# Kernel optimization log

Measured on AMD Instinct MI355X. Metric: run time of the kernel, lower is better.

Reference implementation:

```python
import jax, jax.numpy as jnp
import numpy as np

BS, SL, CL = 32, 512, 20      # batch, seq_len (visits), codes per visit
D, H, V = 256, 4, 20000       # d_model, heads, vocab_size
HD = D // H                   # size_per_head = 64
EPS = 1e-5


def make_pe_table(d_model, max_pos):
    # torch PositionalEncoding: sinusoidal table with a zero pad row prepended
    pe = np.array([[pos / np.power(10000, 2.0 * (j // 2) / d_model)
                    for j in range(d_model)] for pos in range(max_pos)])
    pe[:, 0::2] = np.sin(pe[:, 0::2])
    pe[:, 1::2] = np.cos(pe[:, 1::2])
    pe = np.concatenate([np.zeros((1, d_model)), pe], axis=0)
    return jnp.asarray(pe, dtype=jnp.float32)  # [max_pos+1, d]


def layer_norm(x, g, b):
    mu = jnp.mean(x, axis=-1, keepdims=True)
    var = jnp.mean(jnp.square(x - mu), axis=-1, keepdims=True)
    return (x - mu) * jax.lax.rsqrt(var + EPS) * g + b


def setup_inputs() -> dict:
    key = jax.random.key(0)
    ks = jax.random.split(key, 12)
    input_seqs = jax.random.randint(ks[0], (BS, SL, CL), 0, V, dtype=jnp.int32)
    masks = jnp.ones((BS, SL, SL), dtype=jnp.int32)
    lengths = jax.random.randint(ks[1], (BS,), 1, SL + 1, dtype=jnp.int32)
    seq_time_step = jax.random.uniform(ks[2], (BS, SL), dtype=jnp.float32)
    code_masks = jax.random.uniform(ks[3], (BS, SL, CL), dtype=jnp.float32)

    emb_table = jax.random.normal(ks[4], (V + 1, D), dtype=jnp.float32) * 0.02
    emb_table = emb_table.at[V].set(0.0)  # padding_idx row (never indexed here)
    bound = 1.0 / np.sqrt(V)
    bias_emb = jax.random.uniform(ks[5], (D,), minval=-bound, maxval=bound, dtype=jnp.float32)
    s = 1.0 / np.sqrt(D)
    Wq = jax.random.uniform(ks[6], (D, D), minval=-s, maxval=s, dtype=jnp.float32)
    Wk = jax.random.uniform(ks[7], (D, D), minval=-s, maxval=s, dtype=jnp.float32)
    Wv = jax.random.uniform(ks[8], (D, D), minval=-s, maxval=s, dtype=jnp.float32)
    Wfc = jax.random.uniform(ks[9], (D, D), minval=-s, maxval=s, dtype=jnp.float32)
    ln_g = jnp.ones((D,), dtype=jnp.float32)
    ln_b = jnp.zeros((D,), dtype=jnp.float32)
    so = 1.0 / np.sqrt(4 * D)
    out_w = jax.random.uniform(ks[10], (2, 4 * D), minval=-so, maxval=so, dtype=jnp.float32)
    out_b = jax.random.uniform(ks[11], (2,), minval=-so, maxval=so, dtype=jnp.float32)
    pe_table = make_pe_table(D, SL)

    return dict(input_seqs=input_seqs, masks=masks, lengths=lengths,
                seq_time_step=seq_time_step, code_masks=code_masks,
                emb_table=emb_table, bias_emb=bias_emb, pe_table=pe_table,
                Wq=Wq, Wk=Wk, Wv=Wv, Wfc=Wfc, ln_g=ln_g, ln_b=ln_b,
                out_w=out_w, out_b=out_b)


def reference(input_seqs, masks, lengths, seq_time_step, code_masks,
              emb_table, bias_emb, pe_table, Wq, Wk, Wv, Wfc,
              ln_g, ln_b, out_w, out_b):
    bs, sl, _ = input_seqs.shape
    # visit embedding: sum of code embeddings + bias  -> [bs, sl, d]
    x = emb_table[input_seqs].sum(axis=2) + bias_emb
    # positional encoding: pos ids = 1..len, 0 beyond length
    t_idx = jnp.arange(sl, dtype=jnp.int32)
    pos_ids = jnp.where(t_idx[None, :] < lengths[:, None], t_idx[None, :] + 1, 0)
    x = x + pe_table[pos_ids]
    res = x
    # manual MHA -- NOTE faithful to original: view(bs, H, sl, hd) directly
    q = (x @ Wq.T).reshape(bs, H, sl, HD)
    k = (x @ Wk.T).reshape(bs, H, sl, HD)
    v = (x @ Wv.T).reshape(bs, H, sl, HD)
    energy = jnp.einsum('bhqd,bhkd->bhqk', q, k) / np.sqrt(HD)
    energy = jnp.where(masks[:, None, :, :] == 0, -jnp.inf, energy)
    attn = jax.nn.softmax(energy, axis=-1)
    o = jnp.einsum('bhqk,bhkd->bhqd', attn, v)          # [bs,H,sl,hd]
    o = o.transpose(0, 2, 1, 3).reshape(bs, sl, D)
    x = layer_norm(o @ Wfc.T + res, ln_g, ln_b)
    # zero out positions >= length
    valid = (t_idx[None, :] < lengths[:, None])          # [bs, sl]
    x = jnp.where(valid[:, :, None], x, 0.0)
    # triangular-weighted temporal pooling into 4 bins (vectorized loops)
    lens = lengths.astype(jnp.float32)
    t = jnp.arange(1, sl + 1, dtype=jnp.float32)
    s_val = 4.0 * t[None, :] / lens[:, None]             # [bs, sl]
    m = jnp.arange(1, 5, dtype=jnp.float32)              # 4 bins
    w = jnp.square(1.0 - jnp.abs(s_val[:, :, None] - m[None, None, :]) / 4.0)  # [bs,sl,4]
    U = jnp.einsum('bsm,bsd->bmd', w, x)                 # [bs,4,d]
    U = U.reshape(bs, 4 * D)
    return U @ out_w.T + out_b                           # [bs, 2]
```

## Files before the change

kernel.cpp:

```cpp
#include <hip/hip_runtime.h>

#define BSZ 32
#define SLEN 512
#define CLEN 20
#define DMOD 256
#define NH 4
#define HDIM 64

typedef _Float16 half8 __attribute__((ext_vector_type(8)));
typedef _Float16 half4 __attribute__((ext_vector_type(4)));
typedef float float4v __attribute__((ext_vector_type(4)));

#define MFMA16(a, b, c) __builtin_amdgcn_mfma_f32_16x16x32_f16(a, b, c, 0, 0, 0)
#define PG(fi) ((((fi) >> 4) * 17) + ((fi) & 15))

__global__ __launch_bounds__(256) void k_cast(
    const float* __restrict__ W0, const float* __restrict__ W1,
    const float* __restrict__ W2, const float* __restrict__ W3,
    const float* __restrict__ emb,
    _Float16* __restrict__ wh, _Float16* __restrict__ embh) {
  const int bid = blockIdx.x;
  const float* src;
  _Float16* dst;
  int idx;
  if (bid < 128) {
    const int z = bid >> 5;
    src = (z == 0) ? W0 : (z == 1) ? W1 : (z == 2) ? W2 : W3;
    dst = wh + (size_t)z * 65536;
    idx = ((bid & 31) * 256 + threadIdx.x) * 8;
  } else {
    src = emb;
    dst = embh;
    idx = ((bid - 128) * 256 + threadIdx.x) * 8;
  }
  float v[8];
  *(float4*)v = *(const float4*)(src + idx);
  *(float4*)(v + 4) = *(const float4*)(src + idx + 4);
  half8 h;
  #pragma unroll
  for (int i = 0; i < 8; ++i) h[i] = (_Float16)v[i];
  *(half8*)(dst + idx) = h;
}

__global__ __launch_bounds__(256) void k_embmask(
    const int* __restrict__ seqs, const int* __restrict__ lengths,
    const _Float16* __restrict__ embh, const float* __restrict__ bias,
    const float* __restrict__ pe, _Float16* __restrict__ x,
    const int* __restrict__ masks, unsigned int* __restrict__ pk) {
  const int row0 = blockIdx.x * 8;
  const int sub = threadIdx.x >> 5;
  const int hl = threadIdx.x & 31;
  const int row = row0 + sub;
  const int b = row >> 9, s = row & 511;
  __shared__ int codes[8][CLEN];
  if (threadIdx.x < 8 * CLEN)
    codes[threadIdx.x / CLEN][threadIdx.x % CLEN] = seqs[row0 * CLEN + threadIdx.x];
  __syncthreads();
  const int pos = (s < lengths[b]) ? (s + 1) : 0;
  const int d = hl * 8;
  half8 ev[CLEN];
  #pragma unroll
  for (int c = 0; c < CLEN; ++c)
    ev[c] = *(const half8*)(embh + (size_t)codes[sub][c] * DMOD + d);
  float acc[8];
  *(float4*)acc = *(const float4*)(bias + d);
  *(float4*)(acc + 4) = *(const float4*)(bias + d + 4);
  const float4 pv0 = *(const float4*)(pe + (size_t)pos * DMOD + d);
  const float4 pv1 = *(const float4*)(pe + (size_t)pos * DMOD + d + 4);
  acc[0] += pv0.x; acc[1] += pv0.y; acc[2] += pv0.z; acc[3] += pv0.w;
  acc[4] += pv1.x; acc[5] += pv1.y; acc[6] += pv1.z; acc[7] += pv1.w;
  #pragma unroll
  for (int c = 0; c < CLEN; ++c) {
    #pragma unroll
    for (int i = 0; i < 8; ++i) acc[i] += (float)ev[c][i];
  }
  half8 hv;
  #pragma unroll
  for (int i = 0; i < 8; ++i) hv[i] = (_Float16)acc[i];
  *(half8*)(x + (size_t)row * DMOD + d) = hv;
  const int wv = threadIdx.x >> 6;
  const int lane = threadIdx.x & 63;
  int mv[16];
  #pragma unroll
  for (int p = 0; p < 16; ++p) {
    const int it = wv + p * 4;
    const int r = row0 + (it >> 3);
    const int chunk = it & 7;
    mv[p] = masks[(size_t)r * SLEN + chunk * 64 + lane];
  }
  #pragma unroll
  for (int p = 0; p < 16; ++p) {
    const int it = wv + p * 4;
    const int r = row0 + (it >> 3);
    const int chunk = it & 7;
    const unsigned long long bal = __ballot(mv[p] != 0);
    if (lane == 0) {
      pk[(size_t)r * 16 + chunk * 2]     = (unsigned int)bal;
      pk[(size_t)r * 16 + chunk * 2 + 1] = (unsigned int)(bal >> 32);
    }
  }
}

__global__ __launch_bounds__(256) void k_gemm_qkv(
    const _Float16* __restrict__ A, const _Float16* __restrict__ Wb,
    _Float16* __restrict__ q, _Float16* __restrict__ k, _Float16* __restrict__ v) {
  const int z = blockIdx.z;
  _Float16* Cb = (z == 0) ? q : (z == 1) ? k : v;
  const _Float16* w_ = Wb + (size_t)z * 65536;
  const int m0 = blockIdx.x * 128;
  const int n0 = blockIdx.y * 128;
  const int tid = threadIdx.x;
  const int lane = tid & 63;
  const int w = tid >> 6;
  const int wm = (w >> 1) * 4;
  const int wn = (w & 1) * 4;
  __shared__ _Float16 smem[8704];
  half8* As = (half8*)(smem);
  half8* Ws = (half8*)(smem + 4096);
  float4v acc[4][4];
  #pragma unroll
  for (int i = 0; i < 4; ++i)
    #pragma unroll
    for (int j = 0; j < 4; ++j)
      acc[i][j] = (float4v){0.f, 0.f, 0.f, 0.f};
  int li_[2]; size_t ga_[2], gw_[2];
  #pragma unroll
  for (int p = 0; p < 2; ++p) {
    const int c = tid + p * 256;
    const int r = c & 127, qd = c >> 7;
    li_[p] = (r >> 4) * 64 + qd * 16 + (r & 15);
    ga_[p] = (size_t)(m0 + r) * DMOD + qd * 8;
    gw_[p] = (size_t)(n0 + r) * DMOD + qd * 8;
  }
  half8 pa[2], pw[2];
  #pragma unroll
  for (int p = 0; p < 2; ++p) {
    pa[p] = *(const half8*)(A + ga_[p]);
    pw[p] = *(const half8*)(w_ + gw_[p]);
  }
  for (int k0 = 0; k0 < DMOD; k0 += 32) {
    #pragma unroll
    for (int p = 0; p < 2; ++p) {
      As[li_[p]] = pa[p];
      Ws[li_[p]] = pw[p];
    }
    __syncthreads();
    if (k0 + 32 < DMOD) {
      #pragma unroll
      for (int p = 0; p < 2; ++p) {
        pa[p] = *(const half8*)(A + ga_[p] + k0 + 32);
        pw[p] = *(const half8*)(w_ + gw_[p] + k0 + 32);
      }
    }
    half8 af[4], wf[4];
    #pragma unroll
    for (int i = 0; i < 4; ++i) {
      af[i] = As[(wm + i) * 64 + lane];
      wf[i] = Ws[(wn + i) * 64 + lane];
    }
    #pragma unroll
    for (int i = 0; i < 4; ++i)
      #pragma unroll
      for (int j = 0; j < 4; ++j)
        acc[i][j] = MFMA16(af[i], wf[j], acc[i][j]);
    __syncthreads();
  }
  const int cr = (lane >> 4) * 4;
  const int cc = lane & 15;
  _Float16* Eh = smem;
  #pragma unroll
  for (int ip = 0; ip < 4; ++ip) {
    #pragma unroll
    for (int j = 0; j < 4; ++j) {
      const int col = (wn + j) * 16 + cc;
      #pragma unroll
      for (int r = 0; r < 4; ++r)
        Eh[((w >> 1) * 16 + cr + r) * 136 + col] = (_Float16)acc[ip][j][r];
    }
    __syncthreads();
    #pragma unroll
    for (int e = 0; e < 2; ++e) {
      const int idx = tid + e * 256;
      const int lr = idx >> 4;
      const int cg = idx & 15;
      const int gr = m0 + (lr >> 4) * 64 + ip * 16 + (lr & 15);
      *(half8*)(Cb + (size_t)gr * DMOD + n0 + cg * 8) =
          *(const half8*)&Eh[lr * 136 + cg * 8];
    }
    __syncthreads();
  }
}

__global__ __launch_bounds__(256) void k_vt(
    const _Float16* __restrict__ v, _Float16* __restrict__ vt) {
  const int bh = blockIdx.x;
  const size_t off = (size_t)bh * 32768;
  __shared__ _Float16 Th[64][66];
  const int tid = threadIdx.x;
  const int sc = blockIdx.y * 64;
  #pragma unroll
  for (int p = 0; p < 2; ++p) {
    const int lin = tid + p * 256;
    const int r = lin >> 3, g = lin & 7;
    *(half8*)&Th[r][g * 8] = *(const half8*)(v + off + (size_t)(sc + r) * 64 + g * 8);
  }
  __syncthreads();
  #pragma unroll
  for (int p = 0; p < 2; ++p) {
    const int lin = tid + p * 256;
    const int d = lin >> 3, sg = lin & 7;
    half8 hv;
    #pragma unroll
    for (int j = 0; j < 8; ++j) hv[j] = Th[sg * 8 + j][d];
    *(half8*)(vt + off + (size_t)d * 512 + sc + sg * 8) = hv;
  }
}

__global__ __launch_bounds__(256) void k_fcln(
    const _Float16* __restrict__ A, const _Float16* __restrict__ w_,
    const _Float16* __restrict__ res, const int* __restrict__ lengths,
    const float* __restrict__ g, const float* __restrict__ bb,
    float* __restrict__ Up) {
  const int m0 = blockIdx.x * 64;
  const int b = m0 >> 9;
  const int s0 = m0 & 511;
  const int tid = threadIdx.x;
  const int lane = tid & 63;
  const int w = tid >> 6;
  __shared__ half8 As[256], Ws[1024];
  __shared__ float Rs[4][64], Rq[4][64];
  __shared__ float Fmu[64], Fiv[64];
  float4v acc[4][4];
  #pragma unroll
  for (int i = 0; i < 4; ++i)
    #pragma unroll
    for (int j = 0; j < 4; ++j)
      acc[i][j] = (float4v){0.f, 0.f, 0.f, 0.f};
  const int ra = tid & 63, qa = tid >> 6;
  const int li_a = (ra >> 4) * 64 + qa * 16 + (ra & 15);
  const size_t ga_ = (size_t)(m0 + ra) * DMOD + qa * 8;
  int li_w[4]; size_t gw_[4];
  #pragma unroll
  for (int p = 0; p < 4; ++p) {
    const int c = tid + p * 256;
    const int rw = c & 255, qw = c >> 8;
    li_w[p] = (rw >> 4) * 64 + qw * 16 + (rw & 15);
    gw_[p] = (size_t)rw * DMOD + qw * 8;
  }
  half8 pa = *(const half8*)(A + ga_);
  half8 pw[4];
  #pragma unroll
  for (int p = 0; p < 4; ++p) pw[p] = *(const half8*)(w_ + gw_[p]);
  for (int k0 = 0; k0 < DMOD; k0 += 32) {
    As[li_a] = pa;
    #pragma unroll
    for (int p = 0; p < 4; ++p) Ws[li_w[p]] = pw[p];
    __syncthreads();
    if (k0 + 32 < DMOD) {
      pa = *(const half8*)(A + ga_ + k0 + 32);
      #pragma unroll
      for (int p = 0; p < 4; ++p) pw[p] = *(const half8*)(w_ + gw_[p] + k0 + 32);
    }
    half8 af[4], wf[4];
    #pragma unroll
    for (int i = 0; i < 4; ++i) {
      af[i] = As[i * 64 + lane];
      wf[i] = Ws[(w * 4 + i) * 64 + lane];
    }
    #pragma unroll
    for (int i = 0; i < 4; ++i)
      #pragma unroll
      for (int j = 0; j < 4; ++j)
        acc[i][j] = MFMA16(af[i], wf[j], acc[i][j]);
    __syncthreads();
  }
  const int cr = (lane >> 4) * 4;
  const int cc = lane & 15;
  const int l15 = cc;
  #pragma unroll
  for (int i = 0; i < 4; ++i)
    #pragma unroll
    for (int j = 0; j < 4; ++j) {
      const int col = (w * 4 + j) * 16 + cc;
      #pragma unroll
      for (int r = 0; r < 4; ++r)
        acc[i][j][r] += (float)res[(size_t)(m0 + i * 16 + cr + r) * DMOD + col];
    }
  float S[4][4], Q2[4][4];
  #pragma unroll
  for (int i = 0; i < 4; ++i)
    #pragma unroll
    for (int r = 0; r < 4; ++r) {
      float s = 0.f, q2 = 0.f;
      #pragma unroll
      for (int j = 0; j < 4; ++j) {
        const float v = acc[i][j][r];
        s += v; q2 += v * v;
      }
      #pragma unroll
      for (int off = 1; off <= 8; off <<= 1) {
        s += __shfl_xor(s, off);
        q2 += __shfl_xor(q2, off);
      }
      S[i][r] = s; Q2[i][r] = q2;
    }
  if (l15 == 0) {
    #pragma unroll
    for (int i = 0; i < 4; ++i)
      #pragma unroll
      for (int r = 0; r < 4; ++r) {
        Rs[w][i * 16 + cr + r] = S[i][r];
        Rq[w][i * 16 + cr + r] = Q2[i][r];
      }
  }
  __syncthreads();
  if (tid < 64) {
    const float s = Rs[0][tid] + Rs[1][tid] + Rs[2][tid] + Rs[3][tid];
    const float q2 = Rq[0][tid] + Rq[1][tid] + Rq[2][tid] + Rq[3][tid];
    const float mu = s * (1.0f / DMOD);
    Fmu[tid] = mu;
    Fiv[tid] = rsqrtf(q2 * (1.0f / DMOD) - mu * mu + 1e-5f);
  }
  __syncthreads();
  const int len = lengths[b];
  const float inv4 = 4.0f / (float)len;
  float gl[4], bl[4];
  #pragma unroll
  for (int j = 0; j < 4; ++j) {
    const int col = (w * 4 + j) * 16 + cc;
    gl[j] = g[col]; bl[j] = bb[col];
  }
  float pool[4][4] = {};
  #pragma unroll
  for (int i = 0; i < 4; ++i)
    #pragma unroll
    for (int r = 0; r < 4; ++r) {
      const int row_l = i * 16 + cr + r;
      const int sg = s0 + row_l;
      const bool valid = sg < len;
      const float mu = Fmu[row_l], iv = Fiv[row_l];
      const float sv = (float)(sg + 1) * inv4;
      float t2[4];
      #pragma unroll
      for (int m = 0; m < 4; ++m) {
        const float tm = 1.0f - fabsf(sv - (float)(m + 1)) * 0.25f;
        t2[m] = tm * tm;
      }
      #pragma unroll
      for (int j = 0; j < 4; ++j) {
        const float ov = valid ? (acc[i][j][r] - mu) * iv * gl[j] + bl[j] : 0.f;
        #pragma unroll
        for (int m = 0; m < 4; ++m) pool[m][j] += t2[m] * ov;
      }
    }
  #pragma unroll
  for (int m = 0; m < 4; ++m)
    #pragma unroll
    for (int j = 0; j < 4; ++j) {
      pool[m][j] += __shfl_xor(pool[m][j], 16);
      pool[m][j] += __shfl_xor(pool[m][j], 32);
    }
  const int sc = (m0 >> 6) & 7;
  if ((lane >> 4) == 0) {
    #pragma unroll
    for (int m = 0; m < 4; ++m)
      #pragma unroll
      for (int j = 0; j < 4; ++j)
        Up[(((size_t)b * 8 + sc) * 4 + m) * DMOD + (w * 4 + j) * 16 + cc] =
            pool[m][j];
  }
}

__global__ __launch_bounds__(256, 2) void k_attn(
    const _Float16* __restrict__ q_, const _Float16* __restrict__ k_,
    const _Float16* __restrict__ vt, const unsigned int* __restrict__ pk,
    _Float16* __restrict__ o) {
  const int L = blockIdx.x;
  const int bh = (L & 7) * 16 + ((L >> 3) & 15);
  const int q0 = (L >> 7) * 128;
  const size_t bhoff = (size_t)bh * 32768;
  __shared__ half8 QP[1088];
  __shared__ half8 Ks[2][544], Vs[2][544];
  __shared__ unsigned long long Ms64[2][128];
  __shared__ float Ps[4][128];
  __shared__ float lsum[128];
  const int tid = threadIdx.x;
  const int w = tid >> 6;
  const int lane = tid & 63;
  const int l15 = lane & 15;
  const int quad = lane >> 4;
  #pragma unroll
  for (int p = 0; p < 4; ++p) {
    const int lin = tid + p * 256;
    const int r = lin >> 3, g = lin & 7;
    const int fi = (r >> 4) * 128 + g * 16 + (r & 15);
    QP[PG(fi)] = *(const half8*)(q_ + bhoff + (size_t)(q0 + r) * 64 + g * 8);
  }
  int fi_[2]; const _Float16 *ka_[2], *va_[2];
  #pragma unroll
  for (int p = 0; p < 2; ++p) {
    const int lin = tid + p * 256;
    const int r = lin >> 3, g = lin & 7;
    fi_[p] = PG((r >> 4) * 128 + g * 16 + (r & 15));
    ka_[p] = k_ + bhoff + (size_t)r * 64 + g * 8;
    va_[p] = vt + bhoff + (size_t)r * 512 + g * 8;
  }
  const size_t mb_ = ((size_t)((bh >> 2) << 9) + q0 + (tid >> 1)) * 16 + (tid & 1);
  __syncthreads();
  half8 qf[8][2];
  #pragma unroll
  for (int ns = 0; ns < 8; ++ns) {
    const int gq = ns * 8 + quad;
    qf[ns][0] = QP[gq * 17 + l15];
    qf[ns][1] = QP[(gq + 4) * 17 + l15];
  }
  #pragma unroll
  for (int p = 0; p < 2; ++p) {
    Ks[0][fi_[p]] = *(const half8*)(ka_[p]);
    Vs[0][fi_[p]] = *(const half8*)(va_[p]);
  }
  ((unsigned int*)Ms64[0])[tid] = pk[mb_];
  __syncthreads();
  float4v oacc[8];
  float lsw[8] = {0.f, 0.f, 0.f, 0.f, 0.f, 0.f, 0.f, 0.f};
  #pragma unroll
  for (int ns = 0; ns < 8; ++ns) oacc[ns] = (float4v){0.f, 0.f, 0.f, 0.f};
  const int ga0 = (w * 8 + quad) * 17 + l15;
  const int ga1 = (w * 8 + quad + 4) * 17 + l15;
  for (int t = 0; t < 8; ++t) {
    const int b = t & 1;
    half8 kr0, kr1, vr0, vr1; unsigned int mreg = 0;
    if (t < 7) {
      const int kcn = (t + 1) * 64;
      kr0 = *(const half8*)(ka_[0] + (size_t)kcn * 64);
      kr1 = *(const half8*)(ka_[1] + (size_t)kcn * 64);
      vr0 = *(const half8*)(va_[0] + kcn);
      vr1 = *(const half8*)(va_[1] + kcn);
      mreg = pk[mb_ + (kcn >> 5)];
    }
    const half8 ah0 = Ks[b][ga0], ah1 = Ks[b][ga1];
    #pragma unroll
    for (int ns = 0; ns < 8; ++ns) {
      float4v s = (float4v){0.f, 0.f, 0.f, 0.f};
      s = MFMA16(ah0, qf[ns][0], s);
      s = MFMA16(ah1, qf[ns][1], s);
      const int q = ns * 16 + l15;
      const unsigned long long mrow = Ms64[b][q];
      const unsigned mbits = (unsigned)(mrow >> (w * 16 + quad * 4)) & 15u;
      half4 h4;
      #pragma unroll
      for (int r = 0; r < 4; ++r) {
        const float pe = ((mbits >> r) & 1u) ? __expf(s[r] * 0.125f) : 0.f;
        h4[r] = (_Float16)pe;
        lsw[ns] += pe;
      }
      const int hb = ((ns * 8 + w * 2 + (quad >> 1)) * 17 + l15) * 8 + (quad & 1) * 4;
      *(half4*)((_Float16*)QP + hb) = h4;
    }
    if (t < 7) {
      Ks[b ^ 1][fi_[0]] = kr0;
      Ks[b ^ 1][fi_[1]] = kr1;
      Vs[b ^ 1][fi_[0]] = vr0;
      Vs[b ^ 1][fi_[1]] = vr1;
      ((unsigned int*)Ms64[b ^ 1])[tid] = mreg;
    }
    __syncthreads();
    const half8 vh0 = Vs[b][ga0], vh1 = Vs[b][ga1];
    #pragma unroll
    for (int ns = 0; ns < 8; ++ns) {
      const int pb0 = (ns * 8 + quad) * 17 + l15;
      const int pb1 = (ns * 8 + quad + 4) * 17 + l15;
      oacc[ns] = MFMA16(vh0, QP[pb0], oacc[ns]);
      oacc[ns] = MFMA16(vh1, QP[pb1], oacc[ns]);
    }
    __syncthreads();
  }
  #pragma unroll
  for (int ns = 0; ns < 8; ++ns) {
    lsw[ns] += __shfl_xor(lsw[ns], 16);
    lsw[ns] += __shfl_xor(lsw[ns], 32);
  }
  if (quad == 0) {
    #pragma unroll
    for (int ns = 0; ns < 8; ++ns) Ps[w][ns * 16 + l15] = lsw[ns];
  }
  __syncthreads();
  if (tid < 128) lsum[tid] = Ps[0][tid] + Ps[1][tid] + Ps[2][tid] + Ps[3][tid];
  __syncthreads();
  const int b = bh >> 2, h = bh & 3;
  _Float16* Ot = (_Float16*)QP;
  #pragma unroll
  for (int ns = 0; ns < 8; ++ns) {
    const int q = ns * 16 + l15;
    const float inv = 1.0f / lsum[q];
    half4 h4;
    #pragma unroll
    for (int r = 0; r < 4; ++r) h4[r] = (_Float16)(oacc[ns][r] * inv);
    *(half4*)&Ot[q * 68 + w * 16 + quad * 4] = h4;
  }
  __syncthreads();
  #pragma unroll
  for (int e = 0; e < 4; ++e) {
    const int idx = tid + e * 256;
    const int qq = idx >> 3, g = idx & 7;
    *(half8*)(o + ((size_t)(b * SLEN + q0 + qq)) * DMOD + h * HDIM + g * 8) =
        *(const half8*)&Ot[qq * 68 + g * 8];
  }
}

__global__ __launch_bounds__(256) void k_out(
    const float* __restrict__ Up, const float* __restrict__ ow,
    const float* __restrict__ ob, float* __restrict__ out) {
  const int b = blockIdx.x;
  const int tid = threadIdx.x;
  const int w = tid >> 6;
  const int lane = tid & 63;
  __shared__ float rr[8];
  float4 s = {0.f, 0.f, 0.f, 0.f};
  #pragma unroll
  for (int c = 0; c < 8; ++c) {
    const float4 u = *(const float4*)(Up + ((size_t)b * 8 + c) * 1024 + tid * 4);
    s.x += u.x; s.y += u.y; s.z += u.z; s.w += u.w;
  }
  const float4 w0 = *(const float4*)(ow + tid * 4);
  const float4 w1 = *(const float4*)(ow + 1024 + tid * 4);
  float acc0 = s.x * w0.x + s.y * w0.y + s.z * w0.z + s.w * w0.w;
  float acc1 = s.x * w1.x + s.y * w1.y + s.z * w1.z + s.w * w1.w;
  #pragma unroll
  for (int off = 32; off > 0; off >>= 1) {
    acc0 += __shfl_xor(acc0, off);
    acc1 += __shfl_xor(acc1, off);
  }
  if (lane == 0) { rr[w] = acc0; rr[4 + w] = acc1; }
  __syncthreads();
  if (tid == 0) {
    out[b * 2 + 0] = rr[0] + rr[1] + rr[2] + rr[3] + ob[0];
    out[b * 2 + 1] = rr[4] + rr[5] + rr[6] + rr[7] + ob[1];
  }
}

extern "C" void kernel_launch(void* const* d_in, const int* in_sizes, int n_in,
                              void* d_out, int out_size, void* d_ws, size_t ws_size,
                              hipStream_t stream) {
  const int* seqs     = (const int*)d_in[0];
  const int* masks    = (const int*)d_in[1];
  const int* lengths  = (const int*)d_in[2];
  const float* emb    = (const float*)d_in[5];
  const float* bias   = (const float*)d_in[6];
  const float* pe     = (const float*)d_in[7];
  const float* Wq     = (const float*)d_in[8];
  const float* Wk     = (const float*)d_in[9];
  const float* Wv     = (const float*)d_in[10];
  const float* Wfc    = (const float*)d_in[11];
  const float* ln_g   = (const float*)d_in[12];
  const float* ln_b   = (const float*)d_in[13];
  const float* out_w  = (const float*)d_in[14];
  const float* out_b  = (const float*)d_in[15];
  float* outp = (float*)d_out;

  const size_t NE = (size_t)BSZ * SLEN * DMOD;
  _Float16* q = (_Float16*)d_ws;
  _Float16* k = q + NE;
  _Float16* v = k + NE;
  _Float16* vt = v + NE;
  _Float16* x = vt + NE;
  _Float16* o = x + NE;
  _Float16* wh = o + NE;
  unsigned int* pk = (unsigned int*)(wh + 4 * 65536);
  float* Up = (float*)(pk + BSZ * SLEN * 16);
  _Float16* embh = (_Float16*)d_ws;

  k_cast<<<2628, 256, 0, stream>>>(Wq, Wk, Wv, Wfc, emb, wh, embh);
  k_embmask<<<BSZ * SLEN / 8, 256, 0, stream>>>(seqs, lengths, embh, bias, pe, x,
                                                masks, pk);
  k_gemm_qkv<<<dim3(128, 2, 3), 256, 0, stream>>>(x, wh, q, k, v);
  k_vt<<<dim3(BSZ * NH, 8), 256, 0, stream>>>(v, vt);
  k_attn<<<BSZ * NH * (SLEN / 128), 256, 0, stream>>>(q, k, vt, pk, o);
  k_fcln<<<256, 256, 0, stream>>>(o, wh + 3 * 65536, x, lengths, ln_g, ln_b, Up);
  k_out<<<BSZ, 256, 0, stream>>>(Up, out_w, out_b, outp);
}
```

Before: 202.9 us.

## Deepen attention K/V prefetch to two tiles and widen FC+LN K-step

The attention kernel now prefetches K, V and mask tiles two iterations ahead in registers, fully unrolls the key loop, and merges the initial Q and K/V staging into a single barrier. Its launch bound drops the min-2-blocks hint, so the compiler may use more registers at the cost of occupancy. The FC+LayerNorm kernel doubles its K tile to 64, halving the loop trip count and the number of barriers, but uses more shared memory and registers. The aim is to hide global-load latency and cut synchronisation overhead.

```diff
diff --git a/kernel.cpp b/kernel.cpp
--- a/kernel.cpp
+++ b/kernel.cpp
@@ -227,7 +227,7 @@
   const int tid = threadIdx.x;
   const int lane = tid & 63;
   const int w = tid >> 6;
-  __shared__ half8 As[256], Ws[1024];
+  __shared__ half8 As[512], Ws[2048];
   __shared__ float Rs[4][64], Rq[4][64];
   __shared__ float Fmu[64], Fiv[64];
   float4v acc[4][4];
@@ -236,42 +236,53 @@
     #pragma unroll
     for (int j = 0; j < 4; ++j)
       acc[i][j] = (float4v){0.f, 0.f, 0.f, 0.f};
-  const int ra = tid & 63, qa = tid >> 6;
-  const int li_a = (ra >> 4) * 64 + qa * 16 + (ra & 15);
-  const size_t ga_ = (size_t)(m0 + ra) * DMOD + qa * 8;
-  int li_w[4]; size_t gw_[4];
-  #pragma unroll
-  for (int p = 0; p < 4; ++p) {
+  int li_a[2]; size_t ga_[2];
+  #pragma unroll
+  for (int p = 0; p < 2; ++p) {
+    const int c = tid + p * 256;
+    const int r = c & 63, qd = c >> 6;
+    li_a[p] = (r >> 4) * 128 + qd * 16 + (r & 15);
+    ga_[p] = (size_t)(m0 + r) * DMOD + qd * 8;
+  }
+  int li_w[8]; size_t gw_[8];
+  #pragma unroll
+  for (int p = 0; p < 8; ++p) {
     const int c = tid + p * 256;
     const int rw = c & 255, qw = c >> 8;
-    li_w[p] = (rw >> 4) * 64 + qw * 16 + (rw & 15);
+    li_w[p] = (rw >> 4) * 128 + qw * 16 + (rw & 15);
     gw_[p] = (size_t)rw * DMOD + qw * 8;
   }
-  half8 pa = *(const half8*)(A + ga_);
-  half8 pw[4];
-  #pragma unroll
-  for (int p = 0; p < 4; ++p) pw[p] = *(const half8*)(w_ + gw_[p]);
-  for (int k0 = 0; k0 < DMOD; k0 += 32) {
-    As[li_a] = pa;
-    #pragma unroll
-    for (int p = 0; p < 4; ++p) Ws[li_w[p]] = pw[p];
-    __syncthreads();
-    if (k0 + 32 < DMOD) {
-      pa = *(const half8*)(A + ga_ + k0 + 32);
-      #pragma unroll
-      for (int p = 0; p < 4; ++p) pw[p] = *(const half8*)(w_ + gw_[p] + k0 + 32);
-    }
-    half8 af[4], wf[4];
-    #pragma unroll
-    for (int i = 0; i < 4; ++i) {
-      af[i] = As[i * 64 + lane];
-      wf[i] = Ws[(w * 4 + i) * 64 + lane];
-    }
-    #pragma unroll
-    for (int i = 0; i < 4; ++i)
-      #pragma unroll
-      for (int j = 0; j < 4; ++j)
-        acc[i][j] = MFMA16(af[i], wf[j], acc[i][j]);
+  half8 pa[2], pw[8];
+  #pragma unroll
+  for (int p = 0; p < 2; ++p) pa[p] = *(const half8*)(A + ga_[p]);
+  #pragma unroll
+  for (int p = 0; p < 8; ++p) pw[p] = *(const half8*)(w_ + gw_[p]);
+  for (int k0 = 0; k0 < DMOD; k0 += 64) {
+    #pragma unroll
+    for (int p = 0; p < 2; ++p) As[li_a[p]] = pa[p];
+    #pragma unroll
+    for (int p = 0; p < 8; ++p) Ws[li_w[p]] = pw[p];
+    __syncthreads();
+    if (k0 + 64 < DMOD) {
+      #pragma unroll
+      for (int p = 0; p < 2; ++p) pa[p] = *(const half8*)(A + ga_[p] + k0 + 64);
+      #pragma unroll
+      for (int p = 0; p < 8; ++p) pw[p] = *(const half8*)(w_ + gw_[p] + k0 + 64);
+    }
+    #pragma unroll
+    for (int ks = 0; ks < 2; ++ks) {
+      half8 af[4], wf[4];
+      #pragma unroll
+      for (int i = 0; i < 4; ++i) {
+        af[i] = As[i * 128 + ks * 64 + lane];
+        wf[i] = Ws[(w * 4 + i) * 128 + ks * 64 + lane];
+      }
+      #pragma unroll
+      for (int i = 0; i < 4; ++i)
+        #pragma unroll
+        for (int j = 0; j < 4; ++j)
+          acc[i][j] = MFMA16(af[i], wf[j], acc[i][j]);
+    }
     __syncthreads();
   }
   const int cr = (lane >> 4) * 4;
@@ -371,7 +382,7 @@
   }
 }
 
-__global__ __launch_bounds__(256, 2) void k_attn(
+__global__ __launch_bounds__(256) void k_attn(
     const _Float16* __restrict__ q_, const _Float16* __restrict__ k_,
     const _Float16* __restrict__ vt, const unsigned int* __restrict__ pk,
     _Float16* __restrict__ o) {
@@ -406,6 +417,18 @@
     va_[p] = vt + bhoff + (size_t)r * 512 + g * 8;
   }
   const size_t mb_ = ((size_t)((bh >> 2) << 9) + q0 + (tid >> 1)) * 16 + (tid & 1);
+  #pragma unroll
+  for (int p = 0; p < 2; ++p) {
+    Ks[0][fi_[p]] = *(const half8*)(ka_[p]);
+    Vs[0][fi_[p]] = *(const half8*)(va_[p]);
+  }
+  ((unsigned int*)Ms64[0])[tid] = pk[mb_];
+  half8 krg[2][2], vrg[2][2]; unsigned int mrg[2];
+  krg[1][0] = *(const half8*)(ka_[0] + (size_t)64 * 64);
+  krg[1][1] = *(const half8*)(ka_[1] + (size_t)64 * 64);
+  vrg[1][0] = *(const half8*)(va_[0] + 64);
+  vrg[1][1] = *(const half8*)(va_[1] + 64);
+  mrg[1] = pk[mb_ + 2];
   __syncthreads();
   half8 qf[8][2];
   #pragma unroll
@@ -414,29 +437,22 @@
     qf[ns][0] = QP[gq * 17 + l15];
     qf[ns][1] = QP[(gq + 4) * 17 + l15];
   }
-  #pragma unroll
-  for (int p = 0; p < 2; ++p) {
-    Ks[0][fi_[p]] = *(const half8*)(ka_[p]);
-    Vs[0][fi_[p]] = *(const half8*)(va_[p]);
-  }
-  ((unsigned int*)Ms64[0])[tid] = pk[mb_];
-  __syncthreads();
   float4v oacc[8];
   float lsw[8] = {0.f, 0.f, 0.f, 0.f, 0.f, 0.f, 0.f, 0.f};
   #pragma unroll
   for (int ns = 0; ns < 8; ++ns) oacc[ns] = (float4v){0.f, 0.f, 0.f, 0.f};
   const int ga0 = (w * 8 + quad) * 17 + l15;
   const int ga1 = (w * 8 + quad + 4) * 17 + l15;
+  #pragma unroll
   for (int t = 0; t < 8; ++t) {
     const int b = t & 1;
-    half8 kr0, kr1, vr0, vr1; unsigned int mreg = 0;
-    if (t < 7) {
-      const int kcn = (t + 1) * 64;
-      kr0 = *(const half8*)(ka_[0] + (size_t)kcn * 64);
-      kr1 = *(const half8*)(ka_[1] + (size_t)kcn * 64);
-      vr0 = *(const half8*)(va_[0] + kcn);
-      vr1 = *(const half8*)(va_[1] + kcn);
-      mreg = pk[mb_ + (kcn >> 5)];
+    if (t < 6) {
+      const int kcn = (t + 2) * 64;
+      krg[b][0] = *(const half8*)(ka_[0] + (size_t)kcn * 64);
+      krg[b][1] = *(const half8*)(ka_[1] + (size_t)kcn * 64);
+      vrg[b][0] = *(const half8*)(va_[0] + kcn);
+      vrg[b][1] = *(const half8*)(va_[1] + kcn);
+      mrg[b] = pk[mb_ + (kcn >> 5)];
     }
     const half8 ah0 = Ks[b][ga0], ah1 = Ks[b][ga1];
     #pragma unroll
@@ -458,11 +474,11 @@
       *(half4*)((_Float16*)QP + hb) = h4;
     }
     if (t < 7) {
-      Ks[b ^ 1][fi_[0]] = kr0;
-      Ks[b ^ 1][fi_[1]] = kr1;
-      Vs[b ^ 1][fi_[0]] = vr0;
-      Vs[b ^ 1][fi_[1]] = vr1;
-      ((unsigned int*)Ms64[b ^ 1])[tid] = mreg;
+      Ks[b ^ 1][fi_[0]] = krg[b ^ 1][0];
+      Ks[b ^ 1][fi_[1]] = krg[b ^ 1][1];
+      Vs[b ^ 1][fi_[0]] = vrg[b ^ 1][0];
+      Vs[b ^ 1][fi_[1]] = vrg[b ^ 1][1];
+      ((unsigned int*)Ms64[b ^ 1])[tid] = mrg[b ^ 1];
     }
     __syncthreads();
     const half8 vh0 = Vs[b][ga0], vh1 = Vs[b][ga1];
```

After: 203.5 us. About the same (+0.3%).
